# Performance work log

Hardware: AMD Instinct MI355X
Metric: run time of the kernel (lower is better)

## Reference

```python
import jax, jax.numpy as jnp
import numpy as np

D_MODEL = 4096
NUM_HEADS = 64
DEPTH = D_MODEL // NUM_HEADS  # 64
B = 64   # must equal NUM_HEADS (quirk of original rope-after-split-heads code)
S = 64   # must equal NUM_HEADS (S*DEPTH must equal D_MODEL)


def setup_inputs() -> dict:
    key = jax.random.key(0)
    ks = jax.random.split(key, 9)
    scale = 1.0 / np.sqrt(D_MODEL)
    d = {"x": jax.random.normal(ks[0], (B, S, D_MODEL), dtype=jnp.float32)}
    for i, n in enumerate(["q", "k", "v", "o"]):
        d[f"w_{n}"] = jax.random.normal(ks[1 + i], (D_MODEL, D_MODEL), dtype=jnp.float32) * scale
        d[f"b_{n}"] = jax.random.normal(ks[5 + i], (D_MODEL,), dtype=jnp.float32) * 0.01
    return d


def _rope(x):
    # Faithful to the original: rope is applied to (B, H, S, depth) and treats
    # dim 1 (heads) as the 'sequence' axis, with inv_freq sized for full d_model.
    inv_freq = 1.0 / (10000.0 ** (jnp.arange(0, D_MODEL, 2, dtype=jnp.float32) / D_MODEL))
    pos = jnp.arange(x.shape[1], dtype=jnp.float32)[:, None]       # (H, 1)
    sinusoid = pos * inv_freq                                       # (H, d_model/2)
    sin = jnp.sin(sinusoid)[None, :, None, :]                       # (1, H, 1, d_model/2)
    cos = jnp.cos(sinusoid)[None, :, None, :]
    xr = x.reshape(x.shape[0], x.shape[1], -1, 2)                   # (B, H, S*depth/2, 2)
    real, imag = xr[..., 0], xr[..., 1]                             # (B, H, M) with M == d_model/2
    rot_real = real * cos - imag * sin                              # broadcasts to (1, B, H, M)
    rot_imag = real * sin + imag * cos
    return jnp.stack((rot_real, rot_imag), axis=-1).reshape(x.shape)


def reference(x, w_q, b_q, w_k, b_k, w_v, b_v, w_o, b_o):
    def split_heads(t):  # (B, S, d_model) -> (B, H, S, depth)
        return t.reshape(B, S, NUM_HEADS, DEPTH).transpose(0, 2, 1, 3)

    q = split_heads(x @ w_q.T + b_q)
    k = split_heads(x @ w_k.T + b_k)
    v = split_heads(x @ w_v.T + b_v)
    q = _rope(q)
    k = _rope(k)

    scores = jnp.einsum("bhqd,bhkd->bhqk", q, k) / np.sqrt(DEPTH).astype(np.float32)
    weights = jax.nn.softmax(scores, axis=-1)
    out = jnp.einsum("bhqk,bhkd->bhqd", weights, v)
    out = out.transpose(0, 2, 1, 3).reshape(B, S, D_MODEL)
    return out @ w_o.T + b_o
```

## Files before the change

### kernel.cpp

```cpp
#include <hip/hip_runtime.h>
#include <cstdint>
#include <cstddef>


typedef _Float16 half8 __attribute__((ext_vector_type(8)));
typedef float floatx4 __attribute__((ext_vector_type(4)));

#define NELT_W 16777216u
#define NEG_LOG2_10000_OVER_2048 (-0.0064881408103278559f)

__device__ __forceinline__ void gl_lds16(const void* g, void* l) {
    __builtin_amdgcn_global_load_lds(
        (const __attribute__((address_space(1))) void*)(void*)g,
        (__attribute__((address_space(3))) void*)l,
        16, 0, 0);
}

__global__ __launch_bounds__(256) void cast5_kernel(
    const float* __restrict__ x,  const float* __restrict__ wq,
    const float* __restrict__ wk, const float* __restrict__ wv,
    const float* __restrict__ wo,
    _Float16* __restrict__ xh, _Float16* __restrict__ wcat,
    _Float16* __restrict__ woh)
{
    const float* s;
    _Float16* d;
    switch (blockIdx.y) {
        case 0:  s = x;  d = xh;                 break;
        case 1:  s = wq; d = wcat;               break;
        case 2:  s = wk; d = wcat + NELT_W;      break;
        case 3:  s = wv; d = wcat + 2 * NELT_W;  break;
        default: s = wo; d = woh;                break;
    }
    int i0 = (blockIdx.x * 256 + threadIdx.x) * 8;
    int stride = gridDim.x * 256 * 8;
    for (int i = i0; i < (int)NELT_W; i += stride) {
        const float4 a = *(const float4*)(s + i);
        const float4 b = *(const float4*)(s + i + 4);
        half8 h;
        h[0] = (_Float16)a.x; h[1] = (_Float16)a.y;
        h[2] = (_Float16)a.z; h[3] = (_Float16)a.w;
        h[4] = (_Float16)b.x; h[5] = (_Float16)b.y;
        h[6] = (_Float16)b.z; h[7] = (_Float16)b.w;
        *(half8*)(d + i) = h;
    }
}

__global__ __launch_bounds__(256) void biascat_kernel(
    const float* __restrict__ bq, const float* __restrict__ bk,
    const float* __restrict__ bv, float* __restrict__ out)
{
    int i = blockIdx.x * 256 + threadIdx.x;
    if (i < 4096) {
        out[i]        = bq[i];
        out[4096 + i] = bk[i];
        out[8192 + i] = bv[i];
    }
}


#define STAGE(gb_, lb_, kt_, half_) do {                                      \
    const int R0_ = (half_) << 7;                                             \
    gl_lds16((gb_) + (size_t)R0_ * K + (kt_), (lb_) + R0_ * 64);              \
    gl_lds16((gb_) + (size_t)(R0_ + 64) * K + (kt_), (lb_) + (R0_ + 64) * 64);\
} while (0)

#define LDA(qm_) do {                                                         \
    const _Float16* pa_ = As + bufo + (size_t)(wm + (qm_) * 64 + fr) * 64;    \
    _Pragma("unroll") for (int mt_ = 0; mt_ < 4; ++mt_) {                     \
        af[mt_][0] = *(const half8*)(pa_ + mt_ * 1024 + sw0);                 \
        af[mt_][1] = *(const half8*)(pa_ + mt_ * 1024 + sw1);                 \
    }                                                                         \
} while (0)

#define LDB(qn_, dst_) do {                                                   \
    const _Float16* pb_ = Bs + bufo + (size_t)(wn + (qn_) * 32 + fr) * 64;    \
    _Pragma("unroll") for (int nt_ = 0; nt_ < 2; ++nt_) {                     \
        dst_[nt_][0] = *(const half8*)(pb_ + nt_ * 1024 + sw0);               \
        dst_[nt_][1] = *(const half8*)(pb_ + nt_ * 1024 + sw1);               \
    }                                                                         \
} while (0)

#define MFMAQ(qm_, qn_, bq_) do {                                             \
    _Pragma("unroll") for (int s_ = 0; s_ < 2; ++s_)                          \
    _Pragma("unroll") for (int mt_ = 0; mt_ < 4; ++mt_)                       \
    _Pragma("unroll") for (int nt_ = 0; nt_ < 2; ++nt_)                       \
        acc[(qm_) * 4 + mt_][(qn_) * 2 + nt_] =                               \
            __builtin_amdgcn_mfma_f32_16x16x32_f16(                           \
                af[mt_][s_], bq_[nt_][s_],                                    \
                acc[(qm_) * 4 + mt_][(qn_) * 2 + nt_], 0, 0, 0);              \
} while (0)

#define PHASE_MID()                                                           \
    __builtin_amdgcn_s_barrier();                                             \
    asm volatile("s_waitcnt lgkmcnt(0)");                                     \
    __builtin_amdgcn_sched_barrier(0);                                        \
    __builtin_amdgcn_s_setprio(1)

#define PHASE_END()                                                           \
    __builtin_amdgcn_s_setprio(0);                                            \
    __builtin_amdgcn_s_barrier()

#define TILE() do {                                                           \
    const int ktn_ = (t + 1) << 6;                                            \
    const int kt2_ = (t + 2) << 6;                                            \
    const bool s1_ = (t + 1 < NT);                                            \
    const bool s2_ = (t + 2 < NT);                                            \
           \
    LDA(0); LDB(0, bq0);                                                      \
    if (s1_) STAGE(Ab, AsT + nbufo, ktn_, 0);                                 \
    PHASE_MID();                                                              \
    MFMAQ(0, 0, bq0);                                                         \
    PHASE_END();                                                              \
                           \
    LDB(1, bq1);                                                              \
    if (s1_) STAGE(Ab, AsT + nbufo, ktn_, 1);                                 \
    PHASE_MID();                                                              \
    MFMAQ(0, 1, bq1);                                                         \
    PHASE_END();                                                              \
         \
    LDA(1);                                                                   \
    if (s2_) STAGE(Bb, BsT + bufo, kt2_, 0);                                  \
    PHASE_MID();                                                              \
    MFMAQ(1, 1, bq1);                                                         \
    PHASE_END();                                                              \
            \
    if (s2_) STAGE(Bb, BsT + bufo, kt2_, 1);                                  \
    if (t < NT - 2) asm volatile("s_waitcnt vmcnt(4)");                       \
    else            asm volatile("s_waitcnt vmcnt(0)");                       \
    __builtin_amdgcn_s_barrier();                                             \
    __builtin_amdgcn_sched_barrier(0);                                        \
    __builtin_amdgcn_s_setprio(1);                                            \
    MFMAQ(1, 0, bq0);                                                         \
    PHASE_END();                                                              \
} while (0)

template <int OUT_F16>
__global__ __launch_bounds__(512, 2) void gemm_nt_256(
    const _Float16* __restrict__ A, const _Float16* __restrict__ B,
    const float* __restrict__ bias, void* __restrict__ Cout,
    int M, int N, int K)
{
    __shared__ __align__(16) _Float16 As[2 * 256 * 64];
    __shared__ __align__(16) _Float16 Bs[2 * 256 * 64];

    const int tid = threadIdx.x;
    const int nwg  = gridDim.x;
    const int swz  = (blockIdx.x & 7) * (nwg >> 3) + (blockIdx.x >> 3);
    const int gn   = N >> 8;
    const int row0 = (swz / gn) << 8;
    const int col0 = (swz % gn) << 8;

    const int wave = tid >> 6;
    const int lane = tid & 63;
    const int wm = (wave >> 2) << 7;
    const int wn = (wave & 3) << 6;

    const int fr  = lane & 15;
    const int g4  = lane >> 4;
    const int sw0 = ((g4 ^ (fr & 7)) << 3);
    const int sw1 = (((4 + g4) ^ (fr & 7)) << 3);

    const int srow = tid >> 3;
    const int scol = ((tid & 7) ^ (srow & 7)) << 3;
    const _Float16* Ab = A + (size_t)(row0 + srow) * K + scol;
    const _Float16* Bb = B + (size_t)(col0 + srow) * K + scol;
    _Float16* AsT = As + tid * 8;
    _Float16* BsT = Bs + tid * 8;

    floatx4 acc[8][4];
#pragma unroll
    for (int i = 0; i < 8; i++)
#pragma unroll
        for (int j = 0; j < 4; j++) acc[i][j] = (floatx4){0.f, 0.f, 0.f, 0.f};

    half8 af[4][2], bq0[2][2], bq1[2][2];

    const int NT = K >> 6;

    STAGE(Bb, BsT, 0, 0);
    STAGE(Bb, BsT, 0, 1);
    STAGE(Ab, AsT, 0, 0);
    STAGE(Ab, AsT, 0, 1);
    STAGE(Bb, BsT + 16384, 64, 0);
    STAGE(Bb, BsT + 16384, 64, 1);
    asm volatile("s_waitcnt vmcnt(4)");
    __builtin_amdgcn_s_barrier();

    for (int tt = 0; tt < NT; tt += 2) {
        { const int t = tt;     const int bufo = 0;     const int nbufo = 16384; TILE(); }
        { const int t = tt + 1; const int bufo = 16384; const int nbufo = 0;     TILE(); }
    }

    const int crow = row0 + wm + (g4 << 2);
    const int ccol = col0 + wn + fr;
#pragma unroll
    for (int mi = 0; mi < 8; mi++) {
#pragma unroll
        for (int ni = 0; ni < 4; ni++) {
            const int gc = ccol + ni * 16;
            const float bv = bias[gc];
#pragma unroll
            for (int r2 = 0; r2 < 4; r2++) {
                const int gr = crow + mi * 16 + r2;
                const float v = acc[mi][ni][r2] + bv;
                if (OUT_F16)
                    ((_Float16*)Cout)[(size_t)gr * N + gc] = (_Float16)v;
                else
                    ((float*)Cout)[(size_t)gr * N + gc] = v;
            }
        }
    }
    (void)M;
}

__global__ __launch_bounds__(256) void attn_kernel(
    const _Float16* __restrict__ qkv, _Float16* __restrict__ out)
{
    __shared__ __align__(16) _Float16 qs[64][72];
    __shared__ __align__(16) _Float16 ks[64][72];
    __shared__ __align__(16) _Float16 vt[64][72];
    __shared__ __align__(16) _Float16 ps[4][16][72];

    const int tid  = threadIdx.x;
    const int bb   = blockIdx.x >> 6;
    const int hh   = blockIdx.x & 63;
    const int wave = tid >> 6;
    const int lane = tid & 63;
    const int r  = tid >> 2;
    const int cb = (tid & 3) * 8;
    const float fb = (float)bb;

    const _Float16* grow = qkv + (size_t)(bb * 64 + r) * 12288 + hh * 64;

#pragma unroll
    for (int u = 0; u < 2; u++) {
        const int c8 = cb + u * 32;
        half8 q8 = *(const half8*)(grow + c8);
        half8 k8 = *(const half8*)(grow + 4096 + c8);
        half8 v8 = *(const half8*)(grow + 8192 + c8);
#pragma unroll
        for (int p = 0; p < 4; p++) {
            const int m = r * 32 + (c8 >> 1) + p;
            const float theta = fb * exp2f((float)m * NEG_LOG2_10000_OVER_2048);
            float sn, cs;
            __sincosf(theta, &sn, &cs);
            const float qe = (float)q8[2 * p], qo = (float)q8[2 * p + 1];
            q8[2 * p]     = (_Float16)(qe * cs - qo * sn);
            q8[2 * p + 1] = (_Float16)(qe * sn + qo * cs);
            const float ke = (float)k8[2 * p], ko = (float)k8[2 * p + 1];
            k8[2 * p]     = (_Float16)(ke * cs - ko * sn);
            k8[2 * p + 1] = (_Float16)(ke * sn + ko * cs);
        }
        *(half8*)&qs[r][c8] = q8;
        *(half8*)&ks[r][c8] = k8;
#pragma unroll
        for (int j = 0; j < 8; j++) vt[c8 + j][r] = v8[j];
    }
    __syncthreads();

    const int fr = lane & 15;
    const int fc = (lane >> 4) * 8;

    floatx4 sa[4];
#pragma unroll
    for (int t = 0; t < 4; t++) sa[t] = (floatx4){0.f, 0.f, 0.f, 0.f};
    half8 a0 = *(const half8*)&qs[wave * 16 + fr][fc];
    half8 a1 = *(const half8*)&qs[wave * 16 + fr][fc + 32];
#pragma unroll
    for (int t = 0; t < 4; t++) {
        half8 kb0 = *(const half8*)&ks[t * 16 + fr][fc];
        half8 kb1 = *(const half8*)&ks[t * 16 + fr][fc + 32];
        sa[t] = __builtin_amdgcn_mfma_f32_16x16x32_f16(a0, kb0, sa[t], 0, 0, 0);
        sa[t] = __builtin_amdgcn_mfma_f32_16x16x32_f16(a1, kb1, sa[t], 0, 0, 0);
    }

#pragma unroll
    for (int i = 0; i < 4; i++) {
        float mx = -1e30f;
#pragma unroll
        for (int t = 0; t < 4; t++) mx = fmaxf(mx, sa[t][i]);
#pragma unroll
        for (int d = 1; d < 16; d <<= 1) mx = fmaxf(mx, __shfl_xor(mx, d));
        float sum = 0.f;
        float pv[4];
#pragma unroll
        for (int t = 0; t < 4; t++) {
            const float e = __expf((sa[t][i] - mx) * 0.125f);
            pv[t] = e;
            sum += e;
        }
#pragma unroll
        for (int d = 1; d < 16; d <<= 1) sum += __shfl_xor(sum, d);
        const float inv = 1.0f / sum;
        const int prow = ((lane >> 4) << 2) + i;
#pragma unroll
        for (int t = 0; t < 4; t++)
            ps[wave][prow][t * 16 + fr] = (_Float16)(pv[t] * inv);
    }

    half8 pa0 = *(const half8*)&ps[wave][fr][fc];
    half8 pa1 = *(const half8*)&ps[wave][fr][fc + 32];
    floatx4 oa[4];
#pragma unroll
    for (int t = 0; t < 4; t++) oa[t] = (floatx4){0.f, 0.f, 0.f, 0.f};
#pragma unroll
    for (int t = 0; t < 4; t++) {
        half8 vb0 = *(const half8*)&vt[t * 16 + fr][fc];
        half8 vb1 = *(const half8*)&vt[t * 16 + fr][fc + 32];
        oa[t] = __builtin_amdgcn_mfma_f32_16x16x32_f16(pa0, vb0, oa[t], 0, 0, 0);
        oa[t] = __builtin_amdgcn_mfma_f32_16x16x32_f16(pa1, vb1, oa[t], 0, 0, 0);
    }

    _Float16* obase = out + (size_t)(bb * 64) * 4096 + hh * 64;
#pragma unroll
    for (int t = 0; t < 4; t++)
#pragma unroll
        for (int i = 0; i < 4; i++) {
            const int sq = wave * 16 + ((lane >> 4) << 2) + i;
            obase[(size_t)sq * 4096 + t * 16 + fr] = (_Float16)oa[t][i];
        }
}

extern "C" void kernel_launch(void* const* d_in, const int* in_sizes, int n_in,
                              void* d_out, int out_size, void* d_ws, size_t ws_size,
                              hipStream_t stream)
{
    const float* x  = (const float*)d_in[0];
    const float* wq = (const float*)d_in[1];
    const float* bq = (const float*)d_in[2];
    const float* wk = (const float*)d_in[3];
    const float* bk = (const float*)d_in[4];
    const float* wv = (const float*)d_in[5];
    const float* bv = (const float*)d_in[6];
    const float* wo = (const float*)d_in[7];
    const float* bo = (const float*)d_in[8];

    char* ws = (char*)d_ws;
    _Float16* xh      = (_Float16*)(ws);
    _Float16* wcat    = (_Float16*)(ws + 33554432);
    _Float16* woh     = (_Float16*)(ws + 134217728);
    _Float16* qkv     = (_Float16*)(ws + 167772160);
    _Float16* attnbuf = (_Float16*)(ws + 268435456);
    float*    biascat = (float*)(ws + 301989888);

    cast5_kernel<<<dim3(1024, 5), dim3(256), 0, stream>>>(
        x, wq, wk, wv, wo, xh, wcat, woh);
    biascat_kernel<<<dim3(16), dim3(256), 0, stream>>>(bq, bk, bv, biascat);

    gemm_nt_256<1><<<dim3(768), dim3(512), 0, stream>>>(
        xh, wcat, biascat, qkv, 4096, 12288, 4096);

    attn_kernel<<<dim3(4096), dim3(256), 0, stream>>>(qkv, attnbuf);

    gemm_nt_256<0><<<dim3(256), dim3(512), 0, stream>>>(
        attnbuf, woh, bo, d_out, 4096, 4096, 4096);
}
```

Measured before the change: 843.6 us.

## Restructure GEMM pipeline with quadrant-interleaved warp tiling and cross-tile prefetch

Changes the per-wave output mapping so each wave owns four 64x32 sub-tiles spread across the 256x256 block's quadrants instead of one contiguous 128x64 region. The per-tile schedule is reordered so the LDS fragment reads for the next tile's first quadrant happen at the end of the current tile, overlapping with MFMAs. Global-to-LDS staging is also reshuffled, with a deeper vmcnt wait. The aim is to hide LDS read latency and balance memory traffic across phases. The trade-off is more live registers and a more fragile barrier and wait ordering.

```diff
diff --git a/kernel.cpp b/kernel.cpp
--- a/kernel.cpp
+++ b/kernel.cpp
@@ -65,16 +65,16 @@
     gl_lds16((gb_) + (size_t)(R0_ + 64) * K + (kt_), (lb_) + (R0_ + 64) * 64);\
 } while (0)
 
-#define LDA(qm_) do {                                                         \
-    const _Float16* pa_ = As + bufo + (size_t)(wm + (qm_) * 64 + fr) * 64;    \
-    _Pragma("unroll") for (int mt_ = 0; mt_ < 4; ++mt_) {                     \
+#define LDA2(bo_, ha_, m0_) do {                                              \
+    const _Float16* pa_ = As + (bo_) + (size_t)(((ha_) << 7) + wg2 + fr) * 64;\
+    _Pragma("unroll") for (int mt_ = (m0_); mt_ < (m0_) + 2; ++mt_) {         \
         af[mt_][0] = *(const half8*)(pa_ + mt_ * 1024 + sw0);                 \
         af[mt_][1] = *(const half8*)(pa_ + mt_ * 1024 + sw1);                 \
     }                                                                         \
 } while (0)
 
-#define LDB(qn_, dst_) do {                                                   \
-    const _Float16* pb_ = Bs + bufo + (size_t)(wn + (qn_) * 32 + fr) * 64;    \
+#define LDB4(bo_, hb_, dst_) do {                                             \
+    const _Float16* pb_ = Bs + (bo_) + (size_t)(((hb_) << 7) + wn2 + fr) * 64;\
     _Pragma("unroll") for (int nt_ = 0; nt_ < 2; ++nt_) {                     \
         dst_[nt_][0] = *(const half8*)(pb_ + nt_ * 1024 + sw0);               \
         dst_[nt_][1] = *(const half8*)(pb_ + nt_ * 1024 + sw1);               \
@@ -97,42 +97,44 @@
     __builtin_amdgcn_sched_barrier(0);                                        \
     __builtin_amdgcn_s_setprio(1)
 
-#define PHASE_END()                                                           \
-    __builtin_amdgcn_s_setprio(0);                                            \
-    __builtin_amdgcn_s_barrier()
-
 #define TILE() do {                                                           \
-    const int ktn_ = (t + 1) << 6;                                            \
+    const int kt1_ = (t + 1) << 6;                                            \
     const int kt2_ = (t + 2) << 6;                                            \
     const bool s1_ = (t + 1 < NT);                                            \
     const bool s2_ = (t + 2 < NT);                                            \
-           \
-    LDA(0); LDB(0, bq0);                                                      \
-    if (s1_) STAGE(Ab, AsT + nbufo, ktn_, 0);                                 \
+                       \
+    LDB4(bufo, 1, bq1);                                                       \
+    if (s1_) STAGE(Ab, AsT + nbufo, kt1_, 1);                                 \
     PHASE_MID();                                                              \
     MFMAQ(0, 0, bq0);                                                         \
-    PHASE_END();                                                              \
-                           \
-    LDB(1, bq1);                                                              \
-    if (s1_) STAGE(Ab, AsT + nbufo, ktn_, 1);                                 \
+    __builtin_amdgcn_s_setprio(0);                                            \
+    __builtin_amdgcn_s_barrier();                                             \
+             \
+    if (s2_) STAGE(Ab, AsT + bufo, kt2_, 0);                                  \
     PHASE_MID();                                                              \
     MFMAQ(0, 1, bq1);                                                         \
-    PHASE_END();                                                              \
-         \
-    LDA(1);                                                                   \
+    __builtin_amdgcn_s_setprio(0);                                            \
+    LDA2(bufo, 1, 0);                        \
+    __builtin_amdgcn_s_barrier();                                             \
+       \
+    LDA2(bufo, 1, 2);                                                         \
     if (s2_) STAGE(Bb, BsT + bufo, kt2_, 0);                                  \
     PHASE_MID();                                                              \
+    MFMAQ(1, 0, bq0);                                                         \
+    __builtin_amdgcn_s_setprio(0);                                            \
+    __builtin_amdgcn_s_barrier();                                             \
+     \
+    if (s2_) STAGE(Bb, BsT + bufo, kt2_, 1);                                  \
+    if (t < NT - 2) asm volatile("s_waitcnt vmcnt(6)" ::: "memory");          \
+    else            asm volatile("s_waitcnt vmcnt(0)" ::: "memory");          \
+    __builtin_amdgcn_s_barrier();                                             \
+    __builtin_amdgcn_sched_barrier(0);                                        \
+    if (s1_) LDB4(nbufo, 0, bq0);         \
+    __builtin_amdgcn_s_setprio(1);                                            \
     MFMAQ(1, 1, bq1);                                                         \
-    PHASE_END();                                                              \
-            \
-    if (s2_) STAGE(Bb, BsT + bufo, kt2_, 1);                                  \
-    if (t < NT - 2) asm volatile("s_waitcnt vmcnt(4)");                       \
-    else            asm volatile("s_waitcnt vmcnt(0)");                       \
-    __builtin_amdgcn_s_barrier();                                             \
-    __builtin_amdgcn_sched_barrier(0);                                        \
-    __builtin_amdgcn_s_setprio(1);                                            \
-    MFMAQ(1, 0, bq0);                                                         \
-    PHASE_END();                                                              \
+    __builtin_amdgcn_s_setprio(0);                                            \
+    if (s1_) { LDA2(nbufo, 0, 0); LDA2(nbufo, 0, 2); }          \
+    __builtin_amdgcn_s_barrier();                                             \
 } while (0)
 
 template <int OUT_F16>
@@ -153,8 +155,8 @@
 
     const int wave = tid >> 6;
     const int lane = tid & 63;
-    const int wm = (wave >> 2) << 7;
-    const int wn = (wave & 3) << 6;
+    const int wg2 = (wave >> 2) << 6;
+    const int wn2 = (wave & 3) << 5;
 
     const int fr  = lane & 15;
     const int g4  = lane >> 4;
@@ -178,31 +180,36 @@
 
     const int NT = K >> 6;
 
+    STAGE(Ab, AsT, 0, 0);
+    STAGE(Ab, AsT, 0, 1);
     STAGE(Bb, BsT, 0, 0);
     STAGE(Bb, BsT, 0, 1);
-    STAGE(Ab, AsT, 0, 0);
-    STAGE(Ab, AsT, 0, 1);
+    STAGE(Ab, AsT + 16384, 64, 0);
     STAGE(Bb, BsT + 16384, 64, 0);
     STAGE(Bb, BsT + 16384, 64, 1);
-    asm volatile("s_waitcnt vmcnt(4)");
+    asm volatile("s_waitcnt vmcnt(6)" ::: "memory");
     __builtin_amdgcn_s_barrier();
+    __builtin_amdgcn_sched_barrier(0);
+    LDB4(0, 0, bq0);
+    LDA2(0, 0, 0);
+    LDA2(0, 0, 2);
 
     for (int tt = 0; tt < NT; tt += 2) {
         { const int t = tt;     const int bufo = 0;     const int nbufo = 16384; TILE(); }
         { const int t = tt + 1; const int bufo = 16384; const int nbufo = 0;     TILE(); }
     }
 
-    const int crow = row0 + wm + (g4 << 2);
-    const int ccol = col0 + wn + fr;
+    const int crow = row0 + wg2 + (g4 << 2);
+    const int ccol = col0 + wn2 + fr;
 #pragma unroll
     for (int mi = 0; mi < 8; mi++) {
 #pragma unroll
         for (int ni = 0; ni < 4; ni++) {
-            const int gc = ccol + ni * 16;
+            const int gc = ccol + ((ni >> 1) << 7) + ((ni & 1) << 4);
             const float bv = bias[gc];
 #pragma unroll
             for (int r2 = 0; r2 < 4; r2++) {
-                const int gr = crow + mi * 16 + r2;
+                const int gr = crow + ((mi >> 2) << 7) + ((mi & 3) << 4) + r2;
                 const float v = acc[mi][ni][r2] + bv;
                 if (OUT_F16)
                     ((_Float16*)Cout)[(size_t)gr * N + gc] = (_Float16)v;
```

New measurement: 879.1 us. 4.2% more time.
